# Optimization experiments

Hardware: AMD Instinct MI355X
Metric: run time of the kernel (lower is better)

Reference implementation:

```python
import jax, jax.numpy as jnp
import numpy as np

N_NODES = 50000
IN_NF = 64
HID = 128
OUT_NF = 64
EDGE_HID = HID // 2  # edge_nf_ratio = 2
N_LAYERS = 4
N_EDGES = 800000
NUM_LATENT_NODES = 64
C_EVEN = 1.0
C_ODD = 2.0 / NUM_LATENT_NODES


def setup_inputs() -> dict:
    key = jax.random.key(0)
    ks = jax.random.split(key, 24)
    def lin(k, fan_in, fan_out):
        # torch nn.Linear default init: U(-1/sqrt(fan_in), 1/sqrt(fan_in))
        bound = 1.0 / np.sqrt(fan_in)
        kw, kb = jax.random.split(k)
        w = jax.random.uniform(kw, (fan_in, fan_out), jnp.float32, -bound, bound)
        b = jax.random.uniform(kb, (fan_out,), jnp.float32, -bound, bound)
        return w, b

    h = jax.random.normal(ks[0], (N_NODES, IN_NF), jnp.float32)
    edges_a = jax.random.randint(ks[1], (2, N_EDGES), 0, N_NODES, jnp.int32)
    edges_b = jax.random.randint(ks[2], (2, N_EDGES), 0, N_NODES, jnp.int32)
    update_mask_a = jax.random.randint(ks[3], (N_NODES, 1), 0, 2, jnp.int32).astype(bool)
    update_mask_b = jax.random.randint(ks[4], (N_NODES, 1), 0, 2, jnp.int32).astype(bool)

    emb_in_w, emb_in_b = lin(ks[5], IN_NF, HID)
    emb_out_w, emb_out_b = lin(ks[6], HID, OUT_NF)

    ew1, eb1, ew2, eb2 = [], [], [], []
    nw1, nb1, nw2, nb2 = [], [], [], []
    for i in range(N_LAYERS):
        w, b = lin(ks[7 + i], 2 * HID, EDGE_HID); ew1.append(w); eb1.append(b)
        w, b = lin(ks[11 + i], EDGE_HID, EDGE_HID); ew2.append(w); eb2.append(b)
        w, b = lin(ks[15 + i], HID + EDGE_HID, HID); nw1.append(w); nb1.append(b)
        w, b = lin(ks[19 + i], HID, HID); nw2.append(w); nb2.append(b)

    stack = lambda xs: jnp.stack(xs, 0)
    return {
        "h": h, "edges_a": edges_a, "edges_b": edges_b,
        "update_mask_a": update_mask_a, "update_mask_b": update_mask_b,
        "emb_in_w": emb_in_w, "emb_in_b": emb_in_b,
        "emb_out_w": emb_out_w, "emb_out_b": emb_out_b,
        "edge_w1": stack(ew1), "edge_b1": stack(eb1),
        "edge_w2": stack(ew2), "edge_b2": stack(eb2),
        "node_w1": stack(nw1), "node_b1": stack(nb1),
        "node_w2": stack(nw2), "node_b2": stack(nb2),
    }


def _gcl(h, edges, mask, C, ew1, eb1, ew2, eb2, nw1, nb1, nw2, nb2):
    row, col = edges[0], edges[1]
    # edge model: gather source/target node feats -> 2-layer SiLU MLP
    feat = jnp.concatenate([h[row], h[col]], axis=-1)      # [E, 2*HID]
    m = jax.nn.silu(feat @ ew1 + eb1)                      # [E, EDGE_HID]
    m = jax.nn.silu(m @ ew2 + eb2)                         # [E, EDGE_HID]
    # aggregate messages to receiving nodes (scatter-add), scaled by C
    agg = jax.ops.segment_sum(m, row, num_segments=h.shape[0]) * C
    # node model with residual
    upd = jax.nn.silu(jnp.concatenate([h, agg], axis=-1) @ nw1 + nb1) @ nw2 + nb2
    h_new = h + upd
    # masked asynchronous update: only nodes with mask=True are updated
    return jnp.where(mask, h_new, h)


def reference(h, edges_a, edges_b, update_mask_a, update_mask_b,
              emb_in_w, emb_in_b, emb_out_w, emb_out_b,
              edge_w1, edge_b1, edge_w2, edge_b2,
              node_w1, node_b1, node_w2, node_b2):
    h = h @ emb_in_w + emb_in_b
    for i in range(N_LAYERS):
        if i % 2 == 0:
            edges, mask, C = edges_a, update_mask_a, C_EVEN
        else:
            edges, mask, C = edges_b, update_mask_b, C_ODD
        h = _gcl(h, edges, mask, C,
                 edge_w1[i], edge_b1[i], edge_w2[i], edge_b2[i],
                 node_w1[i], node_b1[i], node_w2[i], node_b2[i])
    h = h @ emb_out_w + emb_out_b
    return h
```

## Files before the change

kernel.cpp:

```cpp
#include <hip/hip_runtime.h>
#include <cstdint>

typedef __bf16 bf16_t;
typedef bf16_t bf16x8 __attribute__((ext_vector_type(8)));
typedef float floatx4 __attribute__((ext_vector_type(4)));
typedef unsigned short ushort4v __attribute__((ext_vector_type(4)));

constexpr int N_NODES = 50000;
constexpr int N_EDGES = 800000;
constexpr int HID = 128;
constexpr int EH = 64;
constexpr int NCH = (N_NODES + 255) / 256;
constexpr int BKT_CAP = 4096;

__device__ __forceinline__ float silu_f(float x) {
    return x * __builtin_amdgcn_rcpf(1.0f + __expf(-x));
}

__global__ __launch_bounds__(256) void pack_all_kernel(
    const float* __restrict__ embin, const float* __restrict__ embout,
    const float* __restrict__ ew1, const float* __restrict__ ew2,
    const float* __restrict__ nw1, const float* __restrict__ nw2,
    bf16_t* __restrict__ pk)
{
    int t = blockIdx.x * 256 + threadIdx.x;
    if (t >= 32768) {
        t -= 32768;
        int lane = t & 63, chunk = t >> 6;
        int ks = chunk & 3, nt = (chunk >> 2) & 7, l = chunk >> 5;
        int quad = lane >> 4, coln = lane & 15;
        const float* Wl = ew1 + l * 256 * 64;
        int kb = (nt >= 4 ? 128 : 0) + ks * 32 + quad * 8;
        int nc = (nt & 3) * 16 + coln;
        bf16x8 v;
#pragma unroll
        for (int j = 0; j < 8; j++) v[j] = (bf16_t)Wl[(kb + j) * 64 + nc];
        *(bf16x8*)(pk + 262144 + t * 8) = v;
        return;
    }
    const float* W; int K, Nc; int base; bf16_t* out;
    if (t < 1024)       { W = embin;  K = 64;  Nc = 128; base = 0;     out = pk; }
    else if (t < 2048)  { W = embout; K = 128; Nc = 64;  base = 1024;  out = pk + 8192; }
    else if (t < 10240) { W = ew1;    K = 256; Nc = 64;  base = 2048;  out = pk + 16384; }
    else if (t < 12288) { W = ew2;    K = 64;  Nc = 64;  base = 10240; out = pk + 81920; }
    else if (t < 24576) { W = nw1;    K = 192; Nc = 128; base = 12288; out = pk + 98304; }
    else                { W = nw2;    K = 128; Nc = 128; base = 24576; out = pk + 196608; }
    t -= base;
    int KS = K >> 5, NT = Nc >> 4;
    int lane = t & 63;
    int chunk = t >> 6;
    int ks = chunk % KS;
    int nt = (chunk / KS) % NT;
    int l  = chunk / (KS * NT);
    int quad = lane >> 4, coln = lane & 15;
    const float* Wl = W + l * K * Nc;
    bf16x8 v;
#pragma unroll
    for (int j = 0; j < 8; j++)
        v[j] = (bf16_t)Wl[(ks * 32 + quad * 8 + j) * Nc + nt * 16 + coln];
    *(bf16x8*)(out + t * 8) = v;
}

__global__ __launch_bounds__(256) void bucketize_kernel(
    const int* __restrict__ ea, const int* __restrict__ eb,
    const int* __restrict__ ma, const int* __restrict__ mb,
    int* __restrict__ gcur, int* __restrict__ gbuf)
{
    int g = blockIdx.y;
    const int* e    = g ? eb : ea;
    const int* mask = g ? mb : ma;
    int* cur = gcur + g * 256;
    int* buf = gbuf + g * 256 * BKT_CAP;
    __shared__ int cnt[256];
    int t = threadIdx.x;
    cnt[t] = 0;
    __syncthreads();
    int base = blockIdx.x * 2048;
    int r[8], c[8]; bool v[8];
#pragma unroll
    for (int k = 0; k < 8; k++) {
        int i = base + k * 256 + t;
        bool ok = i < N_EDGES;
        int ii = ok ? i : 0;
        int rr = e[ii];
        int cc = e[N_EDGES + ii];
        v[k] = ok && (mask[rr] != 0);
        r[k] = rr; c[k] = cc;
        if (v[k]) atomicAdd(&cnt[rr >> 8], 1);
    }
    __syncthreads();
    int lc = cnt[t];
    int gb = 0;
    if (lc > 0) gb = atomicAdd(&cur[t], lc);
    cnt[t] = gb;
    __syncthreads();
#pragma unroll
    for (int k = 0; k < 8; k++) {
        if (v[k]) {
            int bkt = r[k] >> 8;
            int p = atomicAdd(&cnt[bkt], 1);
            if (p < BKT_CAP)
                buf[bkt * BKT_CAP + p] = ((r[k] & 255) << 16) | c[k];
        }
    }
}

__global__ __launch_bounds__(256) void bucket_scan_kernel(
    const int* __restrict__ gcur, int* __restrict__ bases,
    int* __restrict__ mcnt_a, int* __restrict__ mcnt_b)
{
    int g = blockIdx.x;
    const int* cur = gcur + g * 256;
    int t = threadIdx.x, lane = t & 63, wv = t >> 6;
    int v = (t < NCH) ? min(cur[t], BKT_CAP) : 0;
    int s = v;
#pragma unroll
    for (int off = 1; off < 64; off <<= 1) {
        int u = __shfl_up(s, off, 64);
        if (lane >= off) s += u;
    }
    __shared__ int wsum[4];
    if (lane == 63) wsum[wv] = s;
    __syncthreads();
    int woff = 0;
    for (int w = 0; w < wv; w++) woff += wsum[w];
    int excl = s - v + woff;
    bases[g * 256 + t] = excl;
    if (t == NCH - 1) *(g ? mcnt_b : mcnt_a) = excl + v;
}

__global__ __launch_bounds__(256) void bucket_sort_kernel(
    const int* __restrict__ gcur, const int* __restrict__ gbuf,
    const int* __restrict__ bases,
    int* __restrict__ ssrc_a, int* __restrict__ sdst_a,
    int* __restrict__ ssrc_b, int* __restrict__ sdst_b)
{
    int g = blockIdx.y, b = blockIdx.x;
    const int* buf = gbuf + g * 256 * BKT_CAP + b * BKT_CAP;
    int* ssrc = g ? ssrc_b : ssrc_a;
    int* sdst = g ? sdst_b : sdst_a;
    int cnt_e = min(gcur[g * 256 + b], BKT_CAP);
    int base = bases[g * 256 + b];
    __shared__ int h[256];
    __shared__ int wsum[4];
    int t = threadIdx.x, lane = t & 63, wv = t >> 6;
    h[t] = 0;
    __syncthreads();
    int vals[16]; bool vv[16];
#pragma unroll
    for (int k = 0; k < 16; k++) {
        int j = k * 256 + t;
        vv[k] = j < cnt_e;
        int x = vv[k] ? buf[j] : 0;
        vals[k] = x;
        if (vv[k]) atomicAdd(&h[x >> 16], 1);
    }
    __syncthreads();
    int v = h[t];
    int s = v;
#pragma unroll
    for (int off = 1; off < 64; off <<= 1) {
        int u = __shfl_up(s, off, 64);
        if (lane >= off) s += u;
    }
    if (lane == 63) wsum[wv] = s;
    __syncthreads();
    int woff = 0;
    for (int w = 0; w < wv; w++) woff += wsum[w];
    h[t] = s - v + woff;
    __syncthreads();
#pragma unroll
    for (int k = 0; k < 16; k++) {
        if (vv[k]) {
            int x = vals[k];
            int rl = x >> 16, c = x & 0xFFFF;
            int p = atomicAdd(&h[rl], 1);
            int gp = base + p;
            ssrc[gp] = (b << 8) + rl;
            sdst[gp] = c;
        }
    }
}

__global__ __launch_bounds__(256) void scan_phase1(
    const int* __restrict__ bins_a, const int* __restrict__ bins_b,
    int* __restrict__ bs_a, int* __restrict__ bs_b) {
    const int* bins = blockIdx.y ? bins_b : bins_a;
    int* bs = blockIdx.y ? bs_b : bs_a;
    int i = blockIdx.x * 256 + threadIdx.x;
    int v = (i < N_NODES) ? (bins[i] != 0 ? bins[i] : 0) : 0;
#pragma unroll
    for (int off = 32; off; off >>= 1) v += __shfl_down(v, off, 64);
    __shared__ int ws_[4];
    int lane = threadIdx.x & 63, wv = threadIdx.x >> 6;
    if (lane == 0) ws_[wv] = v;
    __syncthreads();
    if (threadIdx.x == 0) bs[blockIdx.x] = ws_[0] + ws_[1] + ws_[2] + ws_[3];
}

__global__ __launch_bounds__(256) void mask_scan2(
    int* __restrict__ ms_a, int* __restrict__ ms_b,
    int* __restrict__ cnt_a, int* __restrict__ cnt_b) {
    int* ms = blockIdx.x ? ms_b : ms_a;
    int* cnt = blockIdx.x ? cnt_b : cnt_a;
    int t = threadIdx.x, lane = t & 63, wv = t >> 6;
    int v = (t < NCH) ? ms[t] : 0;
    int s = v;
#pragma unroll
    for (int off = 1; off < 64; off <<= 1) {
        int u = __shfl_up(s, off, 64);
        if (lane >= off) s += u;
    }
    __shared__ int wsum[4];
    if (lane == 63) wsum[wv] = s;
    __syncthreads();
    int woff = 0;
    for (int w = 0; w < wv; w++) woff += wsum[w];
    int excl = s - v + woff;
    if (t < NCH) ms[t] = excl;
    if (t == NCH - 1) cnt[0] = excl + v;
}

__global__ __launch_bounds__(256) void compact_kernel(
    const int* __restrict__ ma, const int* __restrict__ mb,
    const int* __restrict__ ms_a, const int* __restrict__ ms_b,
    int* __restrict__ la, int* __restrict__ lb) {
    const int* mask = blockIdx.y ? mb : ma;
    const int* ms = blockIdx.y ? ms_b : ms_a;
    int* list = blockIdx.y ? lb : la;
    int i = blockIdx.x * 256 + threadIdx.x;
    int t = threadIdx.x, lane = t & 63, wv = t >> 6;
    int m = (i < N_NODES) ? (mask[i] != 0) : 0;
    unsigned long long bal = __ballot(m != 0);
    int pos = (int)__popcll(bal & ((1ull << lane) - 1ull));
    __shared__ int wsum[4];
    if (lane == 63) wsum[wv] = pos + m;
    __syncthreads();
    int woff = 0;
    for (int w = 0; w < wv; w++) woff += wsum[w];
    if (m) list[ms[blockIdx.x] + woff + pos] = i;
}

__global__ __launch_bounds__(256) void emb_in_kernel(
    const float* __restrict__ h0, const bf16_t* __restrict__ wp,
    const float* __restrict__ bias, float* __restrict__ h, bf16_t* __restrict__ h_bf)
{
    int t = threadIdx.x, wave = t >> 6, lane = t & 63;
    int quad = lane >> 4, col = lane & 15;
    int m0 = blockIdx.x * 64 + wave * 16;
    int ndc = min(m0 + col, N_NODES - 1);
    floatx4 acc[8] = {};
#pragma unroll
    for (int ks = 0; ks < 2; ks++) {
        const float* ap = h0 + ndc * 64 + ks * 32 + quad * 8;
        floatx4 f0 = *(const floatx4*)ap;
        floatx4 f1 = *(const floatx4*)(ap + 4);
        bf16x8 a;
#pragma unroll
        for (int j = 0; j < 4; j++) { a[j] = (bf16_t)f0[j]; a[j + 4] = (bf16_t)f1[j]; }
#pragma unroll
        for (int nt = 0; nt < 8; nt++) {
            bf16x8 b = ((const bf16x8*)wp)[(nt * 2 + ks) * 64 + lane];
            acc[nt] = __builtin_amdgcn_mfma_f32_16x16x32_bf16(a, b, acc[nt], 0, 0, 0);
        }
    }
#pragma unroll
    for (int r = 0; r < 4; r++) {
        int nd2 = m0 + quad * 4 + r;
        if (nd2 < N_NODES) {
#pragma unroll
            for (int nt = 0; nt < 8; nt++) {
                int n = nt * 16 + col;
                float x = acc[nt][r] + bias[n];
                h[nd2 * HID + n] = x;
                h_bf[nd2 * HID + n] = (bf16_t)x;
            }
        }
    }
}

__global__ __launch_bounds__(256) void emb_in_p0_kernel(
    const float* __restrict__ h0, const bf16_t* __restrict__ wp,
    const float* __restrict__ bias, float* __restrict__ h, bf16_t* __restrict__ h_bf,
    const bf16_t* __restrict__ w1cat, const float* __restrict__ b1,
    float* __restrict__ Prow, bf16_t* __restrict__ Pcol)
{
    __shared__ __align__(16) bf16_t hl[4][16 * 136];
    int t = threadIdx.x, wave = t >> 6, lane = t & 63;
    int quad = lane >> 4, col = lane & 15;
    int m0 = blockIdx.x * 64 + wave * 16;
    int ndc = min(m0 + col, N_NODES - 1);
    floatx4 acc[8] = {};
#pragma unroll
    for (int ks = 0; ks < 2; ks++) {
        const float* ap = h0 + ndc * 64 + ks * 32 + quad * 8;
        floatx4 f0 = *(const floatx4*)ap;
        floatx4 f1 = *(const floatx4*)(ap + 4);
        bf16x8 a;
#pragma unroll
        for (int j = 0; j < 4; j++) { a[j] = (bf16_t)f0[j]; a[j + 4] = (bf16_t)f1[j]; }
#pragma unroll
        for (int nt = 0; nt < 8; nt++) {
            bf16x8 b = ((const bf16x8*)wp)[(nt * 2 + ks) * 64 + lane];
            acc[nt] = __builtin_amdgcn_mfma_f32_16x16x32_bf16(a, b, acc[nt], 0, 0, 0);
        }
    }
    bf16_t* myhl = hl[wave];
#pragma unroll
    for (int r = 0; r < 4; r++) {
        int nd2 = m0 + quad * 4 + r;
        bool valid = nd2 < N_NODES;
#pragma unroll
        for (int nt = 0; nt < 8; nt++) {
            int n = nt * 16 + col;
            if (valid) {
                float x = acc[nt][r] + bias[n];
                h[nd2 * HID + n] = x;
                bf16_t hb = (bf16_t)x;
                h_bf[nd2 * HID + n] = hb;
                myhl[(quad * 4 + r) * 136 + n] = hb;
            } else {
                myhl[(quad * 4 + r) * 136 + n] = (bf16_t)0.0f;
            }
        }
    }
    floatx4 accp[8] = {};
#pragma unroll
    for (int ks = 0; ks < 4; ks++) {
        bf16x8 a = *(const bf16x8*)(myhl + col * 136 + ks * 32 + quad * 8);
#pragma unroll
        for (int nt = 0; nt < 8; nt++) {
            bf16x8 b = ((const bf16x8*)w1cat)[(nt * 4 + ks) * 64 + lane];
            accp[nt] = __builtin_amdgcn_mfma_f32_16x16x32_bf16(a, b, accp[nt], 0, 0, 0);
        }
    }
#pragma unroll
    for (int r = 0; r < 4; r++) {
        int nd2 = m0 + quad * 4 + r;
        if (nd2 < N_NODES) {
#pragma unroll
            for (int nt = 0; nt < 4; nt++) {
                int n = nt * 16 + col;
                Prow[nd2 * 64 + n] = accp[nt][r];
                Pcol[nd2 * 64 + n] = (bf16_t)(accp[nt + 4][r] + b1[n]);
            }
        }
    }
}

__global__ __launch_bounds__(256) void pre_edge_kernel(
    const bf16_t* __restrict__ h_bf, const bf16_t* __restrict__ w1cat,
    const float* __restrict__ b1, float* __restrict__ Prow, bf16_t* __restrict__ Pcol)
{
    int t = threadIdx.x, wave = t >> 6, lane = t & 63;
    int quad = lane >> 4, col = lane & 15;
    int m0 = blockIdx.x * 64 + wave * 16;
    int ndc = min(m0 + col, N_NODES - 1);
    floatx4 acc[8] = {};
#pragma unroll
    for (int ks = 0; ks < 4; ks++) {
        bf16x8 a = *(const bf16x8*)(h_bf + ndc * HID + ks * 32 + quad * 8);
#pragma unroll
        for (int nt = 0; nt < 8; nt++) {
            bf16x8 b = ((const bf16x8*)w1cat)[(nt * 4 + ks) * 64 + lane];
            acc[nt] = __builtin_amdgcn_mfma_f32_16x16x32_bf16(a, b, acc[nt], 0, 0, 0);
        }
    }
#pragma unroll
    for (int r = 0; r < 4; r++) {
        int nd2 = m0 + quad * 4 + r;
        if (nd2 < N_NODES) {
#pragma unroll
            for (int nt = 0; nt < 4; nt++) {
                int n = nt * 16 + col;
                Prow[nd2 * 64 + n] = acc[nt][r];
                Pcol[nd2 * 64 + n] = (bf16_t)(acc[nt + 4][r] + b1[n]);
            }
        }
    }
}

__global__ __launch_bounds__(256, 4) void edge_kernel_pre(
    const float* __restrict__ Prow, const bf16_t* __restrict__ Pcol,
    const int* __restrict__ ssrc, const int* __restrict__ sdst,
    const int* __restrict__ m_ptr,
    const bf16_t* __restrict__ w2p, const float* __restrict__ b2,
    float* __restrict__ agg, float C)
{
    __shared__ __align__(16) bf16_t pool[4][64 * 40];

    int t = threadIdx.x;
    int wave = t >> 6, lane = t & 63, quad = lane >> 4, col = lane & 15;
    bf16_t* mbT = pool[wave];

    float b2v[4];
#pragma unroll
    for (int nt = 0; nt < 4; nt++) b2v[nt] = b2[nt * 16 + col];

    int M = m_ptr[0];
    int ntiles = (M + 31) >> 5;
    int wid = blockIdx.x * 4 + wave, nw = gridDim.x * 4;
    if (wid >= ntiles) return;

    int sr = 0x7fffffff, ds = 0x7fffffff;
    { int p = wid * 32 + lane; if (lane < 32 && p < M) { sr = ssrc[p]; ds = sdst[p]; } }

    bf16x8 pcp[2][2];
#pragma unroll
    for (int m = 0; m < 2; m++) {
        int cN = min(__shfl(ds, m * 16 + col, 64), N_NODES - 1);
        const bf16_t* pc = Pcol + cN * 64 + quad * 8;
        pcp[m][0] = *(const bf16x8*)pc;
        pcp[m][1] = *(const bf16x8*)(pc + 32);
    }

    for (int tile = wid; tile < ntiles; tile += nw) {
        int tnc = min(tile + nw, ntiles - 1);
        int srn = 0x7fffffff, dsn = 0x7fffffff;
        { int p = tnc * 32 + lane; if (lane < 32 && p < M) { srn = ssrc[p]; dsn = sdst[p]; } }

        floatx4 acc2[2][4] = {};
#pragma unroll
        for (int m = 0; m < 2; m++) {
            int rN = min(__shfl(sr, m * 16 + col, 64), N_NODES - 1);
            const float* pr = Prow + rN * 64 + quad * 8;
            floatx4 fr[4];
            fr[0] = *(const floatx4*)pr;        fr[1] = *(const floatx4*)(pr + 4);
            fr[2] = *(const floatx4*)(pr + 32); fr[3] = *(const floatx4*)(pr + 36);
#pragma unroll
            for (int ks = 0; ks < 2; ks++) {
                bf16x8 a2;
#pragma unroll
                for (int j = 0; j < 4; j++) {
                    a2[j]     = (bf16_t)silu_f(fr[ks * 2][j]     + (float)pcp[m][ks][j]);
                    a2[j + 4] = (bf16_t)silu_f(fr[ks * 2 + 1][j] + (float)pcp[m][ks][j + 4]);
                }
#pragma unroll
                for (int nt = 0; nt < 4; nt++) {
                    bf16x8 b = ((const bf16x8*)w2p)[(nt * 2 + ks) * 64 + lane];
                    acc2[m][nt] = __builtin_amdgcn_mfma_f32_16x16x32_bf16(a2, b, acc2[m][nt], 0, 0, 0);
                }
            }
        }

        bf16x8 pcn[2][2];
#pragma unroll
        for (int m = 0; m < 2; m++) {
            int cN = min(__shfl(dsn, m * 16 + col, 64), N_NODES - 1);
            const bf16_t* pc = Pcol + cN * 64 + quad * 8;
            pcn[m][0] = *(const bf16x8*)pc;
            pcn[m][1] = *(const bf16x8*)(pc + 32);
        }

#pragma unroll
        for (int m = 0; m < 2; m++)
#pragma unroll
            for (int nt = 0; nt < 4; nt++) {
                ushort4v pv;
#pragma unroll
                for (int r = 0; r < 4; r++) {
                    bf16_t bv = (bf16_t)(silu_f(acc2[m][nt][r] + b2v[nt]) * C);
                    pv[r] = __builtin_bit_cast(unsigned short, bv);
                }
                *(ushort4v*)(mbT + (nt * 16 + col) * 40 + m * 16 + quad * 4) = pv;
            }

        unsigned int bmask;
        {
            int prev = __shfl(sr, lane > 0 ? lane - 1 : 0, 64);
            bmask = (unsigned int)__ballot(lane > 0 && lane < 32 && sr != prev);
        }

        {
            float mv[32];
#pragma unroll
            for (int i = 0; i < 4; i++) {
                bf16x8 v8 = *(const bf16x8*)(mbT + lane * 40 + i * 8);
#pragma unroll
                for (int j = 0; j < 8; j++) mv[i * 8 + j] = (float)v8[j];
            }
            int dp = __shfl(sr, 0, 64);
            float run = mv[0];
#pragma unroll
            for (int r = 1; r < 32; r++) {
                if (bmask & (1u << r)) {
                    if (dp < N_NODES) atomicAdd(agg + dp * EH + lane, run);
                    dp = __shfl(sr, r, 64);
                    run = mv[r];
                } else run += mv[r];
            }
            if (dp < N_NODES) atomicAdd(agg + dp * EH + lane, run);
        }

        sr = srn; ds = dsn;
#pragma unroll
        for (int m = 0; m < 2; m++) {
            pcp[m][0] = pcn[m][0];
            pcp[m][1] = pcn[m][1];
        }
    }
}

__global__ __launch_bounds__(256) void edge_kernel(
    const bf16_t* __restrict__ h_bf, const int* __restrict__ edges,
    const int* __restrict__ mask,
    const bf16_t* __restrict__ w1p, const float* __restrict__ b1,
    const bf16_t* __restrict__ w2p, const float* __restrict__ b2,
    float* __restrict__ agg, float C)
{
    __shared__ __align__(16) bf16_t w1s[16384];
    __shared__ __align__(16) bf16_t w2s[4096];
    __shared__ __align__(16) bf16_t hl[4][16 * 72];

    int t = threadIdx.x;
#pragma unroll
    for (int i = 0; i < 8; i++)
        ((bf16x8*)w1s)[t + 256 * i] = ((const bf16x8*)w1p)[t + 256 * i];
#pragma unroll
    for (int i = 0; i < 2; i++)
        ((bf16x8*)w2s)[t + 256 * i] = ((const bf16x8*)w2p)[t + 256 * i];
    __syncthreads();

    int wave = t >> 6, lane = t & 63, quad = lane >> 4, col = lane & 15;
    bf16_t* myhl = hl[wave];

    float b1v[4], b2v[4];
#pragma unroll
    for (int nt = 0; nt < 4; nt++) { b1v[nt] = b1[nt * 16 + col]; b2v[nt] = b2[nt * 16 + col]; }

    const int ntile_cnt = N_EDGES / 64;
    for (int tile = blockIdx.x; tile < ntile_cnt; tile += gridDim.x) {
        int ebase = tile * 64 + wave * 16;
        int src = edges[ebase + col];
        int dst = edges[N_EDGES + ebase + col];

        floatx4 acc[4] = {};
#pragma unroll
        for (int ks = 0; ks < 8; ks++) {
            int idx = (ks < 4) ? src : dst;
            bf16x8 a = *(const bf16x8*)(h_bf + idx * HID + (ks & 3) * 32 + quad * 8);
#pragma unroll
            for (int nt = 0; nt < 4; nt++) {
                bf16x8 b = ((const bf16x8*)w1s)[(nt * 8 + ks) * 64 + lane];
                acc[nt] = __builtin_amdgcn_mfma_f32_16x16x32_bf16(a, b, acc[nt], 0, 0, 0);
            }
        }
#pragma unroll
        for (int nt = 0; nt < 4; nt++)
#pragma unroll
            for (int r = 0; r < 4; r++)
                myhl[(quad * 4 + r) * 72 + nt * 16 + col] = (bf16_t)silu_f(acc[nt][r] + b1v[nt]);
        __syncthreads();

        floatx4 acc2[4] = {};
#pragma unroll
        for (int ks = 0; ks < 2; ks++) {
            bf16x8 a = *(const bf16x8*)(myhl + col * 72 + ks * 32 + quad * 8);
#pragma unroll
            for (int nt = 0; nt < 4; nt++) {
                bf16x8 b = ((const bf16x8*)w2s)[(nt * 2 + ks) * 64 + lane];
                acc2[nt] = __builtin_amdgcn_mfma_f32_16x16x32_bf16(a, b, acc2[nt], 0, 0, 0);
            }
        }
#pragma unroll
        for (int r = 0; r < 4; r++) {
            int dest = edges[ebase + quad * 4 + r];
            if (mask[dest] != 0) {
                float* aggp = agg + dest * EH;
#pragma unroll
                for (int nt = 0; nt < 4; nt++) {
                    float x = acc2[nt][r] + b2v[nt];
                    atomicAdd(aggp + nt * 16 + col, silu_f(x) * C);
                }
            }
        }
        __syncthreads();
    }
}

__global__ __launch_bounds__(256) void node_kernel_masked(
    float* __restrict__ h, bf16_t* __restrict__ h_bf,
    float* __restrict__ agg, const int* __restrict__ list,
    const int* __restrict__ cnt_ptr,
    const bf16_t* __restrict__ w1p, const float* __restrict__ b1,
    const bf16_t* __restrict__ w2p, const float* __restrict__ b2)
{
    __shared__ __align__(16) bf16_t hl[4][16 * 136];
    int t = threadIdx.x, wave = t >> 6, lane = t & 63;
    int quad = lane >> 4, col = lane & 15;
    int cnt = cnt_ptr[0];
    int m0 = blockIdx.x * 64 + wave * 16;
    if (m0 >= cnt) return;
    int lv = list[min(m0 + col, cnt - 1)];
    int ndc = lv;

    floatx4 acc[8] = {};
#pragma unroll
    for (int ks = 0; ks < 6; ks++) {
        bf16x8 a;
        if (ks < 4) {
            a = *(const bf16x8*)(h_bf + ndc * HID + ks * 32 + quad * 8);
        } else {
            const float* ap = agg + ndc * EH + (ks - 4) * 32 + quad * 8;
            floatx4 f0 = *(const floatx4*)ap;
            floatx4 f1 = *(const floatx4*)(ap + 4);
#pragma unroll
            for (int j = 0; j < 4; j++) { a[j] = (bf16_t)f0[j]; a[j + 4] = (bf16_t)f1[j]; }
        }
#pragma unroll
        for (int nt = 0; nt < 8; nt++) {
            bf16x8 b = ((const bf16x8*)w1p)[(nt * 6 + ks) * 64 + lane];
            acc[nt] = __builtin_amdgcn_mfma_f32_16x16x32_bf16(a, b, acc[nt], 0, 0, 0);
        }
    }
    if ((m0 + col) < cnt) {
        floatx4 z = {0.0f, 0.0f, 0.0f, 0.0f};
        float* zp = agg + ndc * EH + quad * 8;
        *(floatx4*)zp = z; *(floatx4*)(zp + 4) = z;
        *(floatx4*)(zp + 32) = z; *(floatx4*)(zp + 36) = z;
    }
    bf16_t* myhl = hl[wave];
#pragma unroll
    for (int nt = 0; nt < 8; nt++)
#pragma unroll
        for (int r = 0; r < 4; r++) {
            float x = acc[nt][r] + b1[nt * 16 + col];
            myhl[(quad * 4 + r) * 136 + nt * 16 + col] = (bf16_t)silu_f(x);
        }

    floatx4 acc2[8] = {};
#pragma unroll
    for (int ks = 0; ks < 4; ks++) {
        bf16x8 a = *(const bf16x8*)(myhl + col * 136 + ks * 32 + quad * 8);
#pragma unroll
        for (int nt = 0; nt < 8; nt++) {
            bf16x8 b = ((const bf16x8*)w2p)[(nt * 4 + ks) * 64 + lane];
            acc2[nt] = __builtin_amdgcn_mfma_f32_16x16x32_bf16(a, b, acc2[nt], 0, 0, 0);
        }
    }
#pragma unroll
    for (int r = 0; r < 4; r++) {
        if ((m0 + quad * 4 + r) < cnt) {
            int nd2 = __shfl(lv, quad * 4 + r, 64);
#pragma unroll
            for (int nt = 0; nt < 8; nt++) {
                int n = nt * 16 + col;
                float hv = h[nd2 * HID + n] + acc2[nt][r] + b2[n];
                h[nd2 * HID + n] = hv;
                h_bf[nd2 * HID + n] = (bf16_t)hv;
            }
        }
    }
}

__global__ __launch_bounds__(256) void node_kernel(
    float* __restrict__ h, bf16_t* __restrict__ h_bf,
    float* __restrict__ agg, const int* __restrict__ mask,
    const bf16_t* __restrict__ w1p, const float* __restrict__ b1,
    const bf16_t* __restrict__ w2p, const float* __restrict__ b2,
    const bf16_t* __restrict__ wop, const float* __restrict__ bo,
    float* __restrict__ out)
{
    __shared__ __align__(16) bf16_t hl[4][16 * 136];
    int t = threadIdx.x, wave = t >> 6, lane = t & 63;
    int quad = lane >> 4, col = lane & 15;
    int m0 = blockIdx.x * 64 + wave * 16;
    int ndc = min(m0 + col, N_NODES - 1);

    floatx4 acc[8] = {};
#pragma unroll
    for (int ks = 0; ks < 6; ks++) {
        bf16x8 a;
        if (ks < 4) {
            a = *(const bf16x8*)(h_bf + ndc * HID + ks * 32 + quad * 8);
        } else {
            const float* ap = agg + ndc * EH + (ks - 4) * 32 + quad * 8;
            floatx4 f0 = *(const floatx4*)ap;
            floatx4 f1 = *(const floatx4*)(ap + 4);
#pragma unroll
            for (int j = 0; j < 4; j++) { a[j] = (bf16_t)f0[j]; a[j + 4] = (bf16_t)f1[j]; }
        }
#pragma unroll
        for (int nt = 0; nt < 8; nt++) {
            bf16x8 b = ((const bf16x8*)w1p)[(nt * 6 + ks) * 64 + lane];
            acc[nt] = __builtin_amdgcn_mfma_f32_16x16x32_bf16(a, b, acc[nt], 0, 0, 0);
        }
    }
    bf16_t* myhl = hl[wave];
#pragma unroll
    for (int nt = 0; nt < 8; nt++)
#pragma unroll
        for (int r = 0; r < 4; r++) {
            float x = acc[nt][r] + b1[nt * 16 + col];
            myhl[(quad * 4 + r) * 136 + nt * 16 + col] = (bf16_t)silu_f(x);
        }

    floatx4 acc2[8] = {};
#pragma unroll
    for (int ks = 0; ks < 4; ks++) {
        bf16x8 a = *(const bf16x8*)(myhl + col * 136 + ks * 32 + quad * 8);
#pragma unroll
        for (int nt = 0; nt < 8; nt++) {
            bf16x8 b = ((const bf16x8*)w2p)[(nt * 4 + ks) * 64 + lane];
            acc2[nt] = __builtin_amdgcn_mfma_f32_16x16x32_bf16(a, b, acc2[nt], 0, 0, 0);
        }
    }
#pragma unroll
    for (int r = 0; r < 4; r++) {
        int nd2 = m0 + quad * 4 + r;
        bool valid = nd2 < N_NODES;
        bool upd = valid && mask[min(nd2, N_NODES - 1)] != 0;
        if (upd) {
#pragma unroll
            for (int nt = 0; nt < 8; nt++) {
                int n = nt * 16 + col;
                float hv = h[nd2 * HID + n] + acc2[nt][r] + b2[n];
                h[nd2 * HID + n] = hv;
                bf16_t hb = (bf16_t)hv;
                h_bf[nd2 * HID + n] = hb;
                myhl[(quad * 4 + r) * 136 + n] = hb;
            }
        } else {
#pragma unroll
            for (int nt = 0; nt < 8; nt++) {
                int n = nt * 16 + col;
                myhl[(quad * 4 + r) * 136 + n] =
                    valid ? h_bf[nd2 * HID + n] : (bf16_t)0.0f;
            }
        }
    }
    floatx4 ao[4] = {};
#pragma unroll
    for (int ks = 0; ks < 4; ks++) {
        bf16x8 a = *(const bf16x8*)(myhl + col * 136 + ks * 32 + quad * 8);
#pragma unroll
        for (int nt = 0; nt < 4; nt++) {
            bf16x8 b = ((const bf16x8*)wop)[(nt * 4 + ks) * 64 + lane];
            ao[nt] = __builtin_amdgcn_mfma_f32_16x16x32_bf16(a, b, ao[nt], 0, 0, 0);
        }
    }
#pragma unroll
    for (int r = 0; r < 4; r++) {
        int nd2 = m0 + quad * 4 + r;
        if (nd2 < N_NODES) {
#pragma unroll
            for (int nt = 0; nt < 4; nt++) {
                int n = nt * 16 + col;
                out[nd2 * 64 + n] = ao[nt][r] + bo[n];
            }
        }
    }
}

extern "C" void kernel_launch(void* const* d_in, const int* in_sizes, int n_in,
                              void* d_out, int out_size, void* d_ws, size_t ws_size,
                              hipStream_t stream) {
    const float* h0        = (const float*)d_in[0];
    const int*   edges_a   = (const int*)d_in[1];
    const int*   edges_b   = (const int*)d_in[2];
    const int*   mask_a    = (const int*)d_in[3];
    const int*   mask_b    = (const int*)d_in[4];
    const float* emb_in_w  = (const float*)d_in[5];
    const float* emb_in_b  = (const float*)d_in[6];
    const float* emb_out_w = (const float*)d_in[7];
    const float* emb_out_b = (const float*)d_in[8];
    const float* ew1 = (const float*)d_in[9];
    const float* eb1 = (const float*)d_in[10];
    const float* ew2 = (const float*)d_in[11];
    const float* eb2 = (const float*)d_in[12];
    const float* nw1 = (const float*)d_in[13];
    const float* nb1 = (const float*)d_in[14];
    const float* nw2 = (const float*)d_in[15];
    const float* nb2 = (const float*)d_in[16];

    const size_t SZ_H = 25600000, SZ_HBF = 12800000, SZ_AGG = 12800000;
    const size_t SZ_PK = 655360;
    const size_t SZ_S = 3200000, SZ_BS = 1024, SZ_LIST = 200704;
    const size_t SZ_GBUF = (size_t)2 * 256 * BKT_CAP * 4;
    const size_t SZ_PROW = 12800000;
    const size_t SZ_PCOL = 6400000;

    char* ws = (char*)d_ws;
    size_t off = 0;
    float*  h    = (float*)(ws + off);  off += SZ_H;
    bf16_t* h_bf = (bf16_t*)(ws + off); off += SZ_HBF;
    bf16_t* pk   = (bf16_t*)(ws + off); off += SZ_PK;
    int* ssrc_a = (int*)(ws + off); off += SZ_S;
    int* sdst_a = (int*)(ws + off); off += SZ_S;
    int* ssrc_b = (int*)(ws + off); off += SZ_S;
    int* sdst_b = (int*)(ws + off); off += SZ_S;
    int* gbuf   = (int*)(ws + off); off += SZ_GBUF;
    int* gcur   = (int*)(ws + off); off += 2048;
    float* agg  = (float*)(ws + off); off += SZ_AGG;
    int* bases  = (int*)(ws + off); off += 2048;
    int* mcnt_a = (int*)(ws + off); off += 256;
    int* mcnt_b = (int*)(ws + off); off += 256;
    int* ms_a   = (int*)(ws + off); off += SZ_BS;
    int* ms_b   = (int*)(ws + off); off += SZ_BS;
    int* cnt_a  = (int*)(ws + off); off += 256;
    int* cnt_b  = (int*)(ws + off); off += 256;
    int* list_a = (int*)(ws + off); off += SZ_LIST;
    int* list_b = (int*)(ws + off); off += SZ_LIST;
    float*  Prow = (float*)(ws + off);  off += SZ_PROW;
    bf16_t* Pcol = (bf16_t*)(ws + off); off += SZ_PCOL;
    bool ok = (ws_size >= off);

    bf16_t* pk_embin  = pk;
    bf16_t* pk_embout = pk + 8192;
    bf16_t* pk_ew1    = pk + 16384;
    bf16_t* pk_ew2    = pk + 81920;
    bf16_t* pk_nw1    = pk + 98304;
    bf16_t* pk_nw2    = pk + 196608;
    bf16_t* pk_ew1cat = pk + 262144;

    pack_all_kernel<<<160, 256, 0, stream>>>(emb_in_w, emb_out_w, ew1, ew2, nw1, nw2, pk);

    const int node_blocks = (N_NODES + 63) / 64;
    const int bkt_blocks = (N_EDGES + 2047) / 2048;
    if (ok) {
        hipMemsetAsync(gcur, 0, 2048 + SZ_AGG, stream);
        bucketize_kernel<<<dim3(bkt_blocks, 2), 256, 0, stream>>>(
            edges_a, edges_b, mask_a, mask_b, gcur, gbuf);
        bucket_scan_kernel<<<2, 256, 0, stream>>>(gcur, bases, mcnt_a, mcnt_b);
        bucket_sort_kernel<<<dim3(NCH, 2), 256, 0, stream>>>(
            gcur, gbuf, bases, ssrc_a, sdst_a, ssrc_b, sdst_b);
        scan_phase1<<<dim3(NCH, 2), 256, 0, stream>>>(mask_a, mask_b, ms_a, ms_b);
        mask_scan2<<<2, 256, 0, stream>>>(ms_a, ms_b, cnt_a, cnt_b);
        compact_kernel<<<dim3(NCH, 2), 256, 0, stream>>>(mask_a, mask_b, ms_a, ms_b,
                                                         list_a, list_b);
        emb_in_p0_kernel<<<node_blocks, 256, 0, stream>>>(
            h0, pk_embin, emb_in_b, h, h_bf, pk_ew1cat, eb1, Prow, Pcol);
    } else {
        hipMemsetAsync(agg, 0, SZ_AGG, stream);
        emb_in_kernel<<<node_blocks, 256, 0, stream>>>(h0, pk_embin, emb_in_b, h, h_bf);
    }

    for (int l = 0; l < 4; l++) {
        const int* mask = (l & 1) ? mask_b : mask_a;
        float C = (l & 1) ? 0.03125f : 1.0f;
        if (ok) {
            const int* ssrc = (l & 1) ? ssrc_b : ssrc_a;
            const int* sdst = (l & 1) ? sdst_b : sdst_a;
            const int* mp   = (l & 1) ? mcnt_b : mcnt_a;
            if (l > 0)
                pre_edge_kernel<<<node_blocks, 256, 0, stream>>>(
                    h_bf, pk_ew1cat + l * 16384, eb1 + l * 64, Prow, Pcol);
            edge_kernel_pre<<<1024, 256, 0, stream>>>(Prow, Pcol, ssrc, sdst, mp,
                                                      pk_ew2 + l * 4096, eb2 + l * 64,
                                                      agg, C);
        } else {
            const int* edges = (l & 1) ? edges_b : edges_a;
            edge_kernel<<<768, 256, 0, stream>>>(h_bf, edges, mask,
                                                 pk_ew1 + l * 16384, eb1 + l * 64,
                                                 pk_ew2 + l * 4096,  eb2 + l * 64,
                                                 agg, C);
        }
        if (l < 3 && ok) {
            const int* list = (l & 1) ? list_b : list_a;
            const int* cnt  = (l & 1) ? cnt_b : cnt_a;
            node_kernel_masked<<<node_blocks, 256, 0, stream>>>(
                h, h_bf, agg, list, cnt,
                pk_nw1 + l * 24576, nb1 + l * 128,
                pk_nw2 + l * 16384, nb2 + l * 128);
        } else if (l < 3) {
            node_kernel<<<node_blocks, 256, 0, stream>>>(h, h_bf, agg, mask,
                                                         pk_nw1 + l * 24576, nb1 + l * 128,
                                                         pk_nw2 + l * 16384, nb2 + l * 128,
                                                         pk_embout, emb_out_b, (float*)d_out);
            hipMemsetAsync(agg, 0, SZ_AGG, stream);
        } else {
            node_kernel<<<node_blocks, 256, 0, stream>>>(h, h_bf, agg, mask,
                                                         pk_nw1 + 3 * 24576, nb1 + 3 * 128,
                                                         pk_nw2 + 3 * 16384, nb2 + 3 * 128,
                                                         pk_embout, emb_out_b, (float*)d_out);
        }
    }
}
```

Before: 364.2 us.

## Fuse next-layer edge precompute into node kernel and drop mask compaction

Merges the per-layer pre-edge projection (Prow/Pcol for the next layer) into the node update kernel, reusing the freshly updated bf16 node features from shared memory instead of rereading them in a separate launch. Removes the mask scan and compaction kernels; the node kernel now runs over all nodes and branches on the mask per row. This saves several launches and a pass over h_bf, but now spends node-MLP compute on unmasked nodes too.

```diff
diff --git a/kernel.cpp b/kernel.cpp
--- a/kernel.cpp
+++ b/kernel.cpp
@@ -182,65 +182,6 @@
     }
 }
 
-__global__ __launch_bounds__(256) void scan_phase1(
-    const int* __restrict__ bins_a, const int* __restrict__ bins_b,
-    int* __restrict__ bs_a, int* __restrict__ bs_b) {
-    const int* bins = blockIdx.y ? bins_b : bins_a;
-    int* bs = blockIdx.y ? bs_b : bs_a;
-    int i = blockIdx.x * 256 + threadIdx.x;
-    int v = (i < N_NODES) ? (bins[i] != 0 ? bins[i] : 0) : 0;
-#pragma unroll
-    for (int off = 32; off; off >>= 1) v += __shfl_down(v, off, 64);
-    __shared__ int ws_[4];
-    int lane = threadIdx.x & 63, wv = threadIdx.x >> 6;
-    if (lane == 0) ws_[wv] = v;
-    __syncthreads();
-    if (threadIdx.x == 0) bs[blockIdx.x] = ws_[0] + ws_[1] + ws_[2] + ws_[3];
-}
-
-__global__ __launch_bounds__(256) void mask_scan2(
-    int* __restrict__ ms_a, int* __restrict__ ms_b,
-    int* __restrict__ cnt_a, int* __restrict__ cnt_b) {
-    int* ms = blockIdx.x ? ms_b : ms_a;
-    int* cnt = blockIdx.x ? cnt_b : cnt_a;
-    int t = threadIdx.x, lane = t & 63, wv = t >> 6;
-    int v = (t < NCH) ? ms[t] : 0;
-    int s = v;
-#pragma unroll
-    for (int off = 1; off < 64; off <<= 1) {
-        int u = __shfl_up(s, off, 64);
-        if (lane >= off) s += u;
-    }
-    __shared__ int wsum[4];
-    if (lane == 63) wsum[wv] = s;
-    __syncthreads();
-    int woff = 0;
-    for (int w = 0; w < wv; w++) woff += wsum[w];
-    int excl = s - v + woff;
-    if (t < NCH) ms[t] = excl;
-    if (t == NCH - 1) cnt[0] = excl + v;
-}
-
-__global__ __launch_bounds__(256) void compact_kernel(
-    const int* __restrict__ ma, const int* __restrict__ mb,
-    const int* __restrict__ ms_a, const int* __restrict__ ms_b,
-    int* __restrict__ la, int* __restrict__ lb) {
-    const int* mask = blockIdx.y ? mb : ma;
-    const int* ms = blockIdx.y ? ms_b : ms_a;
-    int* list = blockIdx.y ? lb : la;
-    int i = blockIdx.x * 256 + threadIdx.x;
-    int t = threadIdx.x, lane = t & 63, wv = t >> 6;
-    int m = (i < N_NODES) ? (mask[i] != 0) : 0;
-    unsigned long long bal = __ballot(m != 0);
-    int pos = (int)__popcll(bal & ((1ull << lane) - 1ull));
-    __shared__ int wsum[4];
-    if (lane == 63) wsum[wv] = pos + m;
-    __syncthreads();
-    int woff = 0;
-    for (int w = 0; w < wv; w++) woff += wsum[w];
-    if (m) list[ms[blockIdx.x] + woff + pos] = i;
-}
-
 __global__ __launch_bounds__(256) void emb_in_kernel(
     const float* __restrict__ h0, const bf16_t* __restrict__ wp,
     const float* __restrict__ bias, float* __restrict__ h, bf16_t* __restrict__ h_bf)
@@ -348,38 +289,6 @@
     }
 }
 
-__global__ __launch_bounds__(256) void pre_edge_kernel(
-    const bf16_t* __restrict__ h_bf, const bf16_t* __restrict__ w1cat,
-    const float* __restrict__ b1, float* __restrict__ Prow, bf16_t* __restrict__ Pcol)
-{
-    int t = threadIdx.x, wave = t >> 6, lane = t & 63;
-    int quad = lane >> 4, col = lane & 15;
-    int m0 = blockIdx.x * 64 + wave * 16;
-    int ndc = min(m0 + col, N_NODES - 1);
-    floatx4 acc[8] = {};
-#pragma unroll
-    for (int ks = 0; ks < 4; ks++) {
-        bf16x8 a = *(const bf16x8*)(h_bf + ndc * HID + ks * 32 + quad * 8);
-#pragma unroll
-        for (int nt = 0; nt < 8; nt++) {
-            bf16x8 b = ((const bf16x8*)w1cat)[(nt * 4 + ks) * 64 + lane];
-            acc[nt] = __builtin_amdgcn_mfma_f32_16x16x32_bf16(a, b, acc[nt], 0, 0, 0);
-        }
-    }
-#pragma unroll
-    for (int r = 0; r < 4; r++) {
-        int nd2 = m0 + quad * 4 + r;
-        if (nd2 < N_NODES) {
-#pragma unroll
-            for (int nt = 0; nt < 4; nt++) {
-                int n = nt * 16 + col;
-                Prow[nd2 * 64 + n] = acc[nt][r];
-                Pcol[nd2 * 64 + n] = (bf16_t)(acc[nt + 4][r] + b1[n]);
-            }
-        }
-    }
-}
-
 __global__ __launch_bounds__(256, 4) void edge_kernel_pre(
     const float* __restrict__ Prow, const bf16_t* __restrict__ Pcol,
     const int* __restrict__ ssrc, const int* __restrict__ sdst,
@@ -578,21 +487,19 @@
     }
 }
 
-__global__ __launch_bounds__(256) void node_kernel_masked(
+__global__ __launch_bounds__(256) void node_p_kernel(
     float* __restrict__ h, bf16_t* __restrict__ h_bf,
-    float* __restrict__ agg, const int* __restrict__ list,
-    const int* __restrict__ cnt_ptr,
+    float* __restrict__ agg, const int* __restrict__ mask,
     const bf16_t* __restrict__ w1p, const float* __restrict__ b1,
-    const bf16_t* __restrict__ w2p, const float* __restrict__ b2)
+    const bf16_t* __restrict__ w2p, const float* __restrict__ b2,
+    const bf16_t* __restrict__ w1cat, const float* __restrict__ b1n,
+    float* __restrict__ Prow, bf16_t* __restrict__ Pcol)
 {
     __shared__ __align__(16) bf16_t hl[4][16 * 136];
     int t = threadIdx.x, wave = t >> 6, lane = t & 63;
     int quad = lane >> 4, col = lane & 15;
-    int cnt = cnt_ptr[0];
     int m0 = blockIdx.x * 64 + wave * 16;
-    if (m0 >= cnt) return;
-    int lv = list[min(m0 + col, cnt - 1)];
-    int ndc = lv;
+    int ndc = min(m0 + col, N_NODES - 1);
 
     floatx4 acc[8] = {};
 #pragma unroll
@@ -613,11 +520,14 @@
             acc[nt] = __builtin_amdgcn_mfma_f32_16x16x32_bf16(a, b, acc[nt], 0, 0, 0);
         }
     }
-    if ((m0 + col) < cnt) {
-        floatx4 z = {0.0f, 0.0f, 0.0f, 0.0f};
-        float* zp = agg + ndc * EH + quad * 8;
-        *(floatx4*)zp = z; *(floatx4*)(zp + 4) = z;
-        *(floatx4*)(zp + 32) = z; *(floatx4*)(zp + 36) = z;
+    {
+        int nid = m0 + col;
+        if (nid < N_NODES && mask[nid] != 0) {
+            floatx4 z = {0.0f, 0.0f, 0.0f, 0.0f};
+            float* zp = agg + nid * EH + quad * 8;
+            *(floatx4*)zp = z; *(floatx4*)(zp + 4) = z;
+            *(floatx4*)(zp + 32) = z; *(floatx4*)(zp + 36) = z;
+        }
     }
     bf16_t* myhl = hl[wave];
 #pragma unroll
@@ -640,14 +550,47 @@
     }
 #pragma unroll
     for (int r = 0; r < 4; r++) {
-        if ((m0 + quad * 4 + r) < cnt) {
-            int nd2 = __shfl(lv, quad * 4 + r, 64);
+        int nd2 = m0 + quad * 4 + r;
+        bool valid = nd2 < N_NODES;
+        bool upd = valid && mask[min(nd2, N_NODES - 1)] != 0;
+        if (upd) {
 #pragma unroll
             for (int nt = 0; nt < 8; nt++) {
                 int n = nt * 16 + col;
                 float hv = h[nd2 * HID + n] + acc2[nt][r] + b2[n];
                 h[nd2 * HID + n] = hv;
-                h_bf[nd2 * HID + n] = (bf16_t)hv;
+                bf16_t hb = (bf16_t)hv;
+                h_bf[nd2 * HID + n] = hb;
+                myhl[(quad * 4 + r) * 136 + n] = hb;
+            }
+        } else {
+#pragma unroll
+            for (int nt = 0; nt < 8; nt++) {
+                int n = nt * 16 + col;
+                myhl[(quad * 4 + r) * 136 + n] =
+                    valid ? h_bf[nd2 * HID + n] : (bf16_t)0.0f;
+            }
+        }
+    }
+    floatx4 accp[8] = {};
+#pragma unroll
+    for (int ks = 0; ks < 4; ks++) {
+        bf16x8 a = *(const bf16x8*)(myhl + col * 136 + ks * 32 + quad * 8);
+#pragma unroll
+        for (int nt = 0; nt < 8; nt++) {
+            bf16x8 b = ((const bf16x8*)w1cat)[(nt * 4 + ks) * 64 + lane];
+            accp[nt] = __builtin_amdgcn_mfma_f32_16x16x32_bf16(a, b, accp[nt], 0, 0, 0);
+        }
+    }
+#pragma unroll
+    for (int r = 0; r < 4; r++) {
+        int nd2 = m0 + quad * 4 + r;
+        if (nd2 < N_NODES) {
+#pragma unroll
+            for (int nt = 0; nt < 4; nt++) {
+                int n = nt * 16 + col;
+                Prow[nd2 * 64 + n] = accp[nt][r];
+                Pcol[nd2 * 64 + n] = (bf16_t)(accp[nt + 4][r] + b1n[n]);
             }
         }
     }
@@ -775,7 +718,7 @@
 
     const size_t SZ_H = 25600000, SZ_HBF = 12800000, SZ_AGG = 12800000;
     const size_t SZ_PK = 655360;
-    const size_t SZ_S = 3200000, SZ_BS = 1024, SZ_LIST = 200704;
+    const size_t SZ_S = 3200000;
     const size_t SZ_GBUF = (size_t)2 * 256 * BKT_CAP * 4;
     const size_t SZ_PROW = 12800000;
     const size_t SZ_PCOL = 6400000;
@@ -795,12 +738,6 @@
     int* bases  = (int*)(ws + off); off += 2048;
     int* mcnt_a = (int*)(ws + off); off += 256;
     int* mcnt_b = (int*)(ws + off); off += 256;
-    int* ms_a   = (int*)(ws + off); off += SZ_BS;
-    int* ms_b   = (int*)(ws + off); off += SZ_BS;
-    int* cnt_a  = (int*)(ws + off); off += 256;
-    int* cnt_b  = (int*)(ws + off); off += 256;
-    int* list_a = (int*)(ws + off); off += SZ_LIST;
-    int* list_b = (int*)(ws + off); off += SZ_LIST;
     float*  Prow = (float*)(ws + off);  off += SZ_PROW;
     bf16_t* Pcol = (bf16_t*)(ws + off); off += SZ_PCOL;
     bool ok = (ws_size >= off);
@@ -824,10 +761,6 @@
         bucket_scan_kernel<<<2, 256, 0, stream>>>(gcur, bases, mcnt_a, mcnt_b);
         bucket_sort_kernel<<<dim3(NCH, 2), 256, 0, stream>>>(
             gcur, gbuf, bases, ssrc_a, sdst_a, ssrc_b, sdst_b);
-        scan_phase1<<<dim3(NCH, 2), 256, 0, stream>>>(mask_a, mask_b, ms_a, ms_b);
-        mask_scan2<<<2, 256, 0, stream>>>(ms_a, ms_b, cnt_a, cnt_b);
-        compact_kernel<<<dim3(NCH, 2), 256, 0, stream>>>(mask_a, mask_b, ms_a, ms_b,
-                                                         list_a, list_b);
         emb_in_p0_kernel<<<node_blocks, 256, 0, stream>>>(
             h0, pk_embin, emb_in_b, h, h_bf, pk_ew1cat, eb1, Prow, Pcol);
     } else {
@@ -842,37 +775,34 @@
             const int* ssrc = (l & 1) ? ssrc_b : ssrc_a;
             const int* sdst = (l & 1) ? sdst_b : sdst_a;
             const int* mp   = (l & 1) ? mcnt_b : mcnt_a;
-            if (l > 0)
-                pre_edge_kernel<<<node_blocks, 256, 0, stream>>>(
-                    h_bf, pk_ew1cat + l * 16384, eb1 + l * 64, Prow, Pcol);
             edge_kernel_pre<<<1024, 256, 0, stream>>>(Prow, Pcol, ssrc, sdst, mp,
                                                       pk_ew2 + l * 4096, eb2 + l * 64,
                                                       agg, C);
+            if (l < 3) {
+                node_p_kernel<<<node_blocks, 256, 0, stream>>>(
+                    h, h_bf, agg, mask,
+                    pk_nw1 + l * 24576, nb1 + l * 128,
+                    pk_nw2 + l * 16384, nb2 + l * 128,
+                    pk_ew1cat + (l + 1) * 16384, eb1 + (l + 1) * 64,
+                    Prow, Pcol);
+            } else {
+                node_kernel<<<node_blocks, 256, 0, stream>>>(
+                    h, h_bf, agg, mask,
+                    pk_nw1 + 3 * 24576, nb1 + 3 * 128,
+                    pk_nw2 + 3 * 16384, nb2 + 3 * 128,
+                    pk_embout, emb_out_b, (float*)d_out);
+            }
         } else {
             const int* edges = (l & 1) ? edges_b : edges_a;
             edge_kernel<<<768, 256, 0, stream>>>(h_bf, edges, mask,
                                                  pk_ew1 + l * 16384, eb1 + l * 64,
                                                  pk_ew2 + l * 4096,  eb2 + l * 64,
                                                  agg, C);
-        }
-        if (l < 3 && ok) {
-            const int* list = (l & 1) ? list_b : list_a;
-            const int* cnt  = (l & 1) ? cnt_b : cnt_a;
-            node_kernel_masked<<<node_blocks, 256, 0, stream>>>(
-                h, h_bf, agg, list, cnt,
-                pk_nw1 + l * 24576, nb1 + l * 128,
-                pk_nw2 + l * 16384, nb2 + l * 128);
-        } else if (l < 3) {
             node_kernel<<<node_blocks, 256, 0, stream>>>(h, h_bf, agg, mask,
                                                          pk_nw1 + l * 24576, nb1 + l * 128,
                                                          pk_nw2 + l * 16384, nb2 + l * 128,
                                                          pk_embout, emb_out_b, (float*)d_out);
-            hipMemsetAsync(agg, 0, SZ_AGG, stream);
-        } else {
-            node_kernel<<<node_blocks, 256, 0, stream>>>(h, h_bf, agg, mask,
-                                                         pk_nw1 + 3 * 24576, nb1 + 3 * 128,
-                                                         pk_nw2 + 3 * 16384, nb2 + 3 * 128,
-                                                         pk_embout, emb_out_b, (float*)d_out);
-        }
-    }
-}
+            if (l < 3) hipMemsetAsync(agg, 0, SZ_AGG, stream);
+        }
+    }
+}
```

New measurement: 406.3 us. 11.6% more time.
